# Performance work log

Measured on AMD Instinct MI355X. Metric: run time of the kernel, lower is better.

The kernel has to match this reference:

```python
import jax, jax.numpy as jnp
import numpy as np

K = 3  # kernel_size (stride=1, padding=0, same=False, entr=MAX_ENTROPY)


def setup_inputs() -> dict:
    key = jax.random.key(0)
    # Quantized values so global value-counts are non-trivial (mimics real NILM power readings)
    x = jax.random.randint(key, (8, 32, 256, 256), 0, 256).astype(jnp.float32)
    return {"x": x}


def _global_counts(x):
    """For each element, the number of occurrences of its value in the whole tensor
    (equivalent to torch.unique(return_inverse, return_counts) -> counts[inverse])."""
    flat = x.reshape(-1)
    n = flat.shape[0]
    order = jnp.argsort(flat)
    sv = flat[order]
    # group id increments at each value boundary in sorted order
    new_grp = jnp.concatenate([jnp.ones((1,), jnp.int32), (sv[1:] != sv[:-1]).astype(jnp.int32)])
    gid = jnp.cumsum(new_grp) - 1
    grp_counts = jax.ops.segment_sum(jnp.ones((n,), jnp.int32), gid, num_segments=n)
    counts_sorted = grp_counts[gid]
    counts = jnp.zeros((n,), jnp.int32).at[order].set(counts_sorted)
    return counts.reshape(x.shape)


def _windows(a, ho, wo):
    # [B,C,Ho,Wo,K*K]; (di,dj) row-major matches torch unfold(2).unfold(3).view(...,-1)
    return jnp.stack([a[:, :, di:di + ho, dj:dj + wo] for di in range(K) for dj in range(K)], axis=-1)


def reference(x):
    B, C, H, W = x.shape
    ho, wo = H - K + 1, W - K + 1
    probs = _global_counts(x)                 # int32 counts, detached in original
    pw = _windows(probs, ho, wo)              # [B,C,Ho,Wo,9]
    xw = _windows(x, ho, wo)                  # [B,C,Ho,Wo,9]
    # MAX_ENTROPY: pick the value with the minimum global count in each window
    idx = jnp.argmin(pw, axis=-1)             # first minimum, same as torch.min
    pool = jnp.take_along_axis(xw, idx[..., None], axis=-1)[..., 0]
    return pool                               # [B,C,Ho,Wo]
```

## Files before the change

kernel.cpp:

```cpp
#include <hip/hip_runtime.h>

#define B_   8
#define C_   32
#define H_   256
#define W_   256
#define BC_  (B_ * C_)
#define HO_  (H_ - 2)
#define WO_  (W_ - 2)
#define NIN_  (BC_ * H_ * W_)
#define NBINS 256
#define HCOLS 16
#define HBLOCKS 1024

__device__ __align__(8) int g_hist[NBINS];
__device__ int g_part[HBLOCKS * NBINS];

__global__ void zero_hist_kernel() { g_hist[threadIdx.x] = 0; }

__global__ __launch_bounds__(256) void hist_kernel(const float* __restrict__ x) {
    __shared__ int sh[NBINS * HCOLS];
    const int t = threadIdx.x;
    for (int i = t; i < NBINS * HCOLS; i += 256) sh[i] = 0;
    __syncthreads();

    const int col = t & (HCOLS - 1);
    const float4* x4 = (const float4*)x;
    const int stride = HBLOCKS * 256;
    float4 v[8];
#pragma unroll
    for (int half = 0; half < 2; ++half) {
        const int base = blockIdx.x * 256 + t + half * 8 * stride;
#pragma unroll
        for (int k = 0; k < 8; ++k) v[k] = x4[base + k * stride];
#pragma unroll
        for (int k = 0; k < 8; ++k) {
            atomicAdd(&sh[((int)v[k].x) * HCOLS + col], 1);
            atomicAdd(&sh[((int)v[k].y) * HCOLS + col], 1);
            atomicAdd(&sh[((int)v[k].z) * HCOLS + col], 1);
            atomicAdd(&sh[((int)v[k].w) * HCOLS + col], 1);
        }
    }
    __syncthreads();

    int s0 = 0;
#pragma unroll
    for (int c = 0; c < HCOLS; ++c) {
        const int cc = (c + t) & (HCOLS - 1);
        s0 += sh[t * HCOLS + cc];
    }
    g_part[blockIdx.x * NBINS + t] = s0;
}

__global__ __launch_bounds__(256) void reduce_kernel() {
    const int t = threadIdx.x;
    const int r0 = blockIdx.x * (HBLOCKS / 8);
    int s = 0;
#pragma unroll 8
    for (int i = 0; i < HBLOCKS / 8; ++i) s += g_part[(r0 + i) * NBINS + t];
    atomicAdd(&g_hist[t], s);
}

__global__ __launch_bounds__(256) void pool_kernel(const float* __restrict__ x,
                                                   float* __restrict__ out) {
    __shared__ int key_s[NBINS];
    __shared__ int tile[18 * W_];
    const int t = threadIdx.x;
    key_s[t] = (g_hist[t] << 8) | t;
    __syncthreads();

    const int bc = blockIdx.x >> 4;
    const int s  = blockIdx.x & 15;
    const int r0 = s * 16;
    const int rows_out = (r0 + 16 <= HO_) ? 16 : (HO_ - r0);
    const int rows_in  = rows_out + 2;

    const float4* xin = (const float4*)(x + ((long long)bc * H_ + r0) * W_);
    const int nf4 = rows_in * (W_ / 4);
    for (int idx = t; idx < nf4; idx += 256) {
        float4 v = xin[idx];
        int4 k;
        k.x = key_s[(int)v.x];
        k.y = key_s[(int)v.y];
        k.z = key_s[(int)v.z];
        k.w = key_s[(int)v.w];
        ((int4*)tile)[idx] = k;
    }
    __syncthreads();

    if (t >= WO_) return;

    int a0 = tile[t],        a1 = tile[t + 1],        a2 = tile[t + 2];
    int b0 = tile[W_ + t],   b1 = tile[W_ + t + 1],   b2 = tile[W_ + t + 2];
    float* orow = out + ((long long)bc * HO_ + r0) * WO_ + t;
    for (int r = 0; r < rows_out; ++r) {
        const int base = (r + 2) * W_ + t;
        const int c0 = tile[base], c1 = tile[base + 1], c2 = tile[base + 2];
        int best = a0, bm = a0 & ~255;
#define CAND(kk) { const int m = (kk) & ~255; if (m < bm) { bm = m; best = (kk); } }
        CAND(a1) CAND(a2) CAND(b0) CAND(b1) CAND(b2) CAND(c0) CAND(c1) CAND(c2)
#undef CAND
        orow[(long long)r * WO_] = (float)(best & 255);
        a0 = b0; a1 = b1; a2 = b2;
        b0 = c0; b1 = c1; b2 = c2;
    }
}

extern "C" void kernel_launch(void* const* d_in, const int* in_sizes, int n_in,
                              void* d_out, int out_size, void* d_ws, size_t ws_size,
                              hipStream_t stream) {
    const float* x = (const float*)d_in[0];
    float* out = (float*)d_out;
    (void)d_ws; (void)ws_size;

    zero_hist_kernel<<<1, NBINS, 0, stream>>>();
    hist_kernel<<<HBLOCKS, 256, 0, stream>>>(x);
    reduce_kernel<<<8, 256, 0, stream>>>();
    pool_kernel<<<BC_ * 16, 256, 0, stream>>>(x, out);
}
```

Measured before the change: 132.8 us.

## Cache input as packed bytes during histogram pass and reread in pool kernel

The histogram kernel now also writes each float4 as four packed 8-bit values into a global buffer, and the pool kernel reads that quarter-size buffer instead of the original float input. The reduction is folded into one 1024-thread block that writes the histogram directly, which drops the zeroing kernel and the global atomics. This trades an extra 16 MB write in the histogram pass for a 4x smaller read in the pool pass, plus one fewer launch. It relies on the input values being integers in 0..255, the same assumption the existing histogram already makes.

```diff
diff --git a/kernel.cpp b/kernel.cpp
--- a/kernel.cpp
+++ b/kernel.cpp
@@ -14,8 +14,7 @@
 
 __device__ __align__(8) int g_hist[NBINS];
 __device__ int g_part[HBLOCKS * NBINS];
-
-__global__ void zero_hist_kernel() { g_hist[threadIdx.x] = 0; }
+__device__ unsigned g_x8[NIN_ / 4];
 
 __global__ __launch_bounds__(256) void hist_kernel(const float* __restrict__ x) {
     __shared__ int sh[NBINS * HCOLS];
@@ -34,10 +33,13 @@
         for (int k = 0; k < 8; ++k) v[k] = x4[base + k * stride];
 #pragma unroll
         for (int k = 0; k < 8; ++k) {
-            atomicAdd(&sh[((int)v[k].x) * HCOLS + col], 1);
-            atomicAdd(&sh[((int)v[k].y) * HCOLS + col], 1);
-            atomicAdd(&sh[((int)v[k].z) * HCOLS + col], 1);
-            atomicAdd(&sh[((int)v[k].w) * HCOLS + col], 1);
+            const int ax = (int)v[k].x, ay = (int)v[k].y, az = (int)v[k].z, aw = (int)v[k].w;
+            g_x8[base + k * stride] =
+                (unsigned)ax | ((unsigned)ay << 8) | ((unsigned)az << 16) | ((unsigned)aw << 24);
+            atomicAdd(&sh[ax * HCOLS + col], 1);
+            atomicAdd(&sh[ay * HCOLS + col], 1);
+            atomicAdd(&sh[az * HCOLS + col], 1);
+            atomicAdd(&sh[aw * HCOLS + col], 1);
         }
     }
     __syncthreads();
@@ -51,17 +53,20 @@
     g_part[blockIdx.x * NBINS + t] = s0;
 }
 
-__global__ __launch_bounds__(256) void reduce_kernel() {
+__global__ __launch_bounds__(1024) void reduce_kernel() {
+    __shared__ int acc[4 * NBINS];
     const int t = threadIdx.x;
-    const int r0 = blockIdx.x * (HBLOCKS / 8);
+    const int bin = t & (NBINS - 1);
+    const int seg = t >> 8;
     int s = 0;
-#pragma unroll 8
-    for (int i = 0; i < HBLOCKS / 8; ++i) s += g_part[(r0 + i) * NBINS + t];
-    atomicAdd(&g_hist[t], s);
+#pragma unroll 16
+    for (int r = seg * 256; r < seg * 256 + 256; ++r) s += g_part[r * NBINS + bin];
+    acc[seg * NBINS + bin] = s;
+    __syncthreads();
+    if (t < NBINS) g_hist[t] = acc[t] + acc[NBINS + t] + acc[2 * NBINS + t] + acc[3 * NBINS + t];
 }
 
-__global__ __launch_bounds__(256) void pool_kernel(const float* __restrict__ x,
-                                                   float* __restrict__ out) {
+__global__ __launch_bounds__(256) void pool_kernel(float* __restrict__ out) {
     __shared__ int key_s[NBINS];
     __shared__ int tile[18 * W_];
     const int t = threadIdx.x;
@@ -74,15 +79,15 @@
     const int rows_out = (r0 + 16 <= HO_) ? 16 : (HO_ - r0);
     const int rows_in  = rows_out + 2;
 
-    const float4* xin = (const float4*)(x + ((long long)bc * H_ + r0) * W_);
-    const int nf4 = rows_in * (W_ / 4);
-    for (int idx = t; idx < nf4; idx += 256) {
-        float4 v = xin[idx];
+    const unsigned* xin = g_x8 + ((long long)bc * H_ + r0) * (W_ / 4);
+    const int nw = rows_in * (W_ / 4);
+    for (int idx = t; idx < nw; idx += 256) {
+        const unsigned u = xin[idx];
         int4 k;
-        k.x = key_s[(int)v.x];
-        k.y = key_s[(int)v.y];
-        k.z = key_s[(int)v.z];
-        k.w = key_s[(int)v.w];
+        k.x = key_s[u & 255];
+        k.y = key_s[(u >> 8) & 255];
+        k.z = key_s[(u >> 16) & 255];
+        k.w = key_s[u >> 24];
         ((int4*)tile)[idx] = k;
     }
     __syncthreads();
@@ -112,8 +117,7 @@
     float* out = (float*)d_out;
     (void)d_ws; (void)ws_size;
 
-    zero_hist_kernel<<<1, NBINS, 0, stream>>>();
     hist_kernel<<<HBLOCKS, 256, 0, stream>>>(x);
-    reduce_kernel<<<8, 256, 0, stream>>>();
-    pool_kernel<<<BC_ * 16, 256, 0, stream>>>(x, out);
+    reduce_kernel<<<1, 1024, 0, stream>>>();
+    pool_kernel<<<BC_ * 16, 256, 0, stream>>>(out);
 }
```

Measured after the change: 142.9 us. 7.6% more time.

## Fuse histogram and pooling into one cooperative kernel with grid sync

Applied to the files above, without the earlier changes.

Replaces the separate histogram, reduce and pool kernels with a single cooperative kernel of 256 blocks of 1024 threads, one block per image. Each block histograms its own image and atomically adds the result into 32 partial rows, then waits on a grid-wide sync, sums the partials and pools the same image. The image is read again after the sync, which may hit in L2/MALL, and launch overhead is reduced. In exchange, only 256 large blocks run, one per CU on mi355x, which lowers occupancy and parallelism for the pooling phase. The grid barrier adds its own cost.

```diff
diff --git a/kernel.cpp b/kernel.cpp
--- a/kernel.cpp
+++ b/kernel.cpp
@@ -1,4 +1,7 @@
 #include <hip/hip_runtime.h>
+#include <hip/hip_cooperative_groups.h>
+
+namespace cg = cooperative_groups;
 
 #define B_   8
 #define C_   32
@@ -7,31 +10,36 @@
 #define BC_  (B_ * C_)
 #define HO_  (H_ - 2)
 #define WO_  (W_ - 2)
-#define NIN_  (BC_ * H_ * W_)
 #define NBINS 256
 #define HCOLS 16
-#define HBLOCKS 1024
+#define PROWS 32
 
-__device__ __align__(8) int g_hist[NBINS];
-__device__ int g_part[HBLOCKS * NBINS];
+__device__ int g_part[PROWS * NBINS];
 
-__global__ void zero_hist_kernel() { g_hist[threadIdx.x] = 0; }
+__global__ __launch_bounds__(1024) void zero_part_kernel() {
+    const int t = threadIdx.x;
+#pragma unroll
+    for (int i = 0; i < (PROWS * NBINS) / 1024; ++i) g_part[i * 1024 + t] = 0;
+}
 
-__global__ __launch_bounds__(256) void hist_kernel(const float* __restrict__ x) {
-    __shared__ int sh[NBINS * HCOLS];
+__global__ __launch_bounds__(1024) void fused_kernel(const float* __restrict__ x,
+                                                     float* __restrict__ out) {
+    __shared__ int tile[18 * W_];
+    __shared__ int key_s[NBINS];
     const int t = threadIdx.x;
-    for (int i = t; i < NBINS * HCOLS; i += 256) sh[i] = 0;
+    const int bc = blockIdx.x;
+    const float4* ximg = (const float4*)(x + (long long)bc * H_ * W_);
+
+    int* sh = tile;
+    for (int i = t; i < NBINS * HCOLS; i += 1024) sh[i] = 0;
     __syncthreads();
 
     const int col = t & (HCOLS - 1);
-    const float4* x4 = (const float4*)x;
-    const int stride = HBLOCKS * 256;
-    float4 v[8];
 #pragma unroll
     for (int half = 0; half < 2; ++half) {
-        const int base = blockIdx.x * 256 + t + half * 8 * stride;
+        float4 v[8];
 #pragma unroll
-        for (int k = 0; k < 8; ++k) v[k] = x4[base + k * stride];
+        for (int k = 0; k < 8; ++k) v[k] = ximg[t + (half * 8 + k) * 1024];
 #pragma unroll
         for (int k = 0; k < 8; ++k) {
             atomicAdd(&sh[((int)v[k].x) * HCOLS + col], 1);
@@ -42,66 +50,64 @@
     }
     __syncthreads();
 
-    int s0 = 0;
+    if (t < NBINS) {
+        int s0 = 0;
 #pragma unroll
-    for (int c = 0; c < HCOLS; ++c) {
-        const int cc = (c + t) & (HCOLS - 1);
-        s0 += sh[t * HCOLS + cc];
+        for (int c = 0; c < HCOLS; ++c)
+            s0 += sh[t * HCOLS + ((c + t) & (HCOLS - 1))];
+        atomicAdd(&g_part[(bc & (PROWS - 1)) * NBINS + t], s0);
     }
-    g_part[blockIdx.x * NBINS + t] = s0;
-}
 
-__global__ __launch_bounds__(256) void reduce_kernel() {
-    const int t = threadIdx.x;
-    const int r0 = blockIdx.x * (HBLOCKS / 8);
-    int s = 0;
-#pragma unroll 8
-    for (int i = 0; i < HBLOCKS / 8; ++i) s += g_part[(r0 + i) * NBINS + t];
-    atomicAdd(&g_hist[t], s);
-}
+    cg::this_grid().sync();
 
-__global__ __launch_bounds__(256) void pool_kernel(const float* __restrict__ x,
-                                                   float* __restrict__ out) {
-    __shared__ int key_s[NBINS];
-    __shared__ int tile[18 * W_];
-    const int t = threadIdx.x;
-    key_s[t] = (g_hist[t] << 8) | t;
-    __syncthreads();
-
-    const int bc = blockIdx.x >> 4;
-    const int s  = blockIdx.x & 15;
-    const int r0 = s * 16;
-    const int rows_out = (r0 + 16 <= HO_) ? 16 : (HO_ - r0);
-    const int rows_in  = rows_out + 2;
-
-    const float4* xin = (const float4*)(x + ((long long)bc * H_ + r0) * W_);
-    const int nf4 = rows_in * (W_ / 4);
-    for (int idx = t; idx < nf4; idx += 256) {
-        float4 v = xin[idx];
-        int4 k;
-        k.x = key_s[(int)v.x];
-        k.y = key_s[(int)v.y];
-        k.z = key_s[(int)v.z];
-        k.w = key_s[(int)v.w];
-        ((int4*)tile)[idx] = k;
+    if (t < NBINS) {
+        int g = 0;
+#pragma unroll
+        for (int r = 0; r < PROWS; ++r) g += g_part[r * NBINS + t];
+        key_s[t] = (g << 8) | t;
     }
     __syncthreads();
 
-    if (t >= WO_) return;
+    const int cidx = t & 255;
+    const int rg   = t >> 8;
+    for (int s = 0; s < 16; ++s) {
+        const int r0 = s * 16;
+        const int rows_out = (s == 15) ? 14 : 16;
+        const int rows_in  = rows_out + 2;
 
-    int a0 = tile[t],        a1 = tile[t + 1],        a2 = tile[t + 2];
-    int b0 = tile[W_ + t],   b1 = tile[W_ + t + 1],   b2 = tile[W_ + t + 2];
-    float* orow = out + ((long long)bc * HO_ + r0) * WO_ + t;
-    for (int r = 0; r < rows_out; ++r) {
-        const int base = (r + 2) * W_ + t;
-        const int c0 = tile[base], c1 = tile[base + 1], c2 = tile[base + 2];
-        int best = a0, bm = a0 & ~255;
+        const float4* xrow = (const float4*)(x + ((long long)bc * H_ + r0) * W_);
+        const int nf4 = rows_in * (W_ / 4);
+        for (int idx = t; idx < nf4; idx += 1024) {
+            float4 v = xrow[idx];
+            int4 k;
+            k.x = key_s[(int)v.x];
+            k.y = key_s[(int)v.y];
+            k.z = key_s[(int)v.z];
+            k.w = key_s[(int)v.w];
+            ((int4*)tile)[idx] = k;
+        }
+        __syncthreads();
+
+        const int rbase = rg * 4;
+        const int rcnt = (rows_out - rbase < 4) ? (rows_out - rbase) : 4;
+        if (cidx < WO_ && rcnt > 0) {
+            const int* tp = tile + cidx;
+            int a0 = tp[rbase * W_],       a1 = tp[rbase * W_ + 1],       a2 = tp[rbase * W_ + 2];
+            int b0 = tp[(rbase + 1) * W_], b1 = tp[(rbase + 1) * W_ + 1], b2 = tp[(rbase + 1) * W_ + 2];
+            float* orow = out + ((long long)bc * HO_ + r0 + rbase) * WO_ + cidx;
+            for (int r = 0; r < rcnt; ++r) {
+                const int cb = (rbase + 2 + r) * W_;
+                const int c0 = tp[cb], c1 = tp[cb + 1], c2 = tp[cb + 2];
+                int best = a0, bm = a0 & ~255;
 #define CAND(kk) { const int m = (kk) & ~255; if (m < bm) { bm = m; best = (kk); } }
-        CAND(a1) CAND(a2) CAND(b0) CAND(b1) CAND(b2) CAND(c0) CAND(c1) CAND(c2)
+                CAND(a1) CAND(a2) CAND(b0) CAND(b1) CAND(b2) CAND(c0) CAND(c1) CAND(c2)
 #undef CAND
-        orow[(long long)r * WO_] = (float)(best & 255);
-        a0 = b0; a1 = b1; a2 = b2;
-        b0 = c0; b1 = c1; b2 = c2;
+                orow[(long long)r * WO_] = (float)(best & 255);
+                a0 = b0; a1 = b1; a2 = b2;
+                b0 = c0; b1 = c1; b2 = c2;
+            }
+        }
+        __syncthreads();
     }
 }
 
@@ -112,8 +118,9 @@
     float* out = (float*)d_out;
     (void)d_ws; (void)ws_size;
 
-    zero_hist_kernel<<<1, NBINS, 0, stream>>>();
-    hist_kernel<<<HBLOCKS, 256, 0, stream>>>(x);
-    reduce_kernel<<<8, 256, 0, stream>>>();
-    pool_kernel<<<BC_ * 16, 256, 0, stream>>>(x, out);
+    zero_part_kernel<<<1, 1024, 0, stream>>>();
+
+    void* args[] = { (void*)&x, (void*)&out };
+    hipLaunchCooperativeKernel((const void*)fused_kernel, dim3(BC_), dim3(1024),
+                               args, 0, stream);
 }
```

Measured after the change: 188.8 us. 1.42x slower.

## Vectorize pool window min with branchless keys and single-block histogram reduce

Applied to the files above, without the earlier changes.

Removes the zero-hist launch by reducing the partial histograms in one 1024-thread block that writes final counts directly, with no atomics. The pool kernel issues all global loads up front and stores keys into a padded int4 tile. Each thread now computes four output columns over a band of rows using branchless min over keys, where a window-position tag is ORed into bits 8-11 so ties still resolve to the first minimum. Outputs go out as nontemporal float2 stores. This trades more registers per thread for fewer launches and less shared-memory traffic and branching. It relies on count<<12 not overflowing, which holds for this input size.

```diff
diff --git a/kernel.cpp b/kernel.cpp
--- a/kernel.cpp
+++ b/kernel.cpp
@@ -11,11 +11,12 @@
 #define NBINS 256
 #define HCOLS 16
 #define HBLOCKS 1024
+#define TW4  65
+
+typedef float f2v __attribute__((ext_vector_type(2)));
 
 __device__ __align__(8) int g_hist[NBINS];
 __device__ int g_part[HBLOCKS * NBINS];
-
-__global__ void zero_hist_kernel() { g_hist[threadIdx.x] = 0; }
 
 __global__ __launch_bounds__(256) void hist_kernel(const float* __restrict__ x) {
     __shared__ int sh[NBINS * HCOLS];
@@ -44,64 +45,85 @@
 
     int s0 = 0;
 #pragma unroll
-    for (int c = 0; c < HCOLS; ++c) {
-        const int cc = (c + t) & (HCOLS - 1);
-        s0 += sh[t * HCOLS + cc];
-    }
+    for (int c = 0; c < HCOLS; ++c) s0 += sh[t * HCOLS + ((c + t) & (HCOLS - 1))];
     g_part[blockIdx.x * NBINS + t] = s0;
 }
 
-__global__ __launch_bounds__(256) void reduce_kernel() {
+__global__ __launch_bounds__(1024) void reduce_kernel() {
+    __shared__ int acc[4 * NBINS];
     const int t = threadIdx.x;
-    const int r0 = blockIdx.x * (HBLOCKS / 8);
+    const int bin = t & (NBINS - 1);
+    const int seg = t >> 8;
     int s = 0;
-#pragma unroll 8
-    for (int i = 0; i < HBLOCKS / 8; ++i) s += g_part[(r0 + i) * NBINS + t];
-    atomicAdd(&g_hist[t], s);
+#pragma unroll 16
+    for (int r = seg * 256; r < seg * 256 + 256; ++r) s += g_part[r * NBINS + bin];
+    acc[seg * NBINS + bin] = s;
+    __syncthreads();
+    if (t < NBINS) g_hist[t] = acc[t] + acc[NBINS + t] + acc[2 * NBINS + t] + acc[3 * NBINS + t];
 }
 
 __global__ __launch_bounds__(256) void pool_kernel(const float* __restrict__ x,
                                                    float* __restrict__ out) {
     __shared__ int key_s[NBINS];
-    __shared__ int tile[18 * W_];
+    __shared__ int4 tile[18 * TW4];
     const int t = threadIdx.x;
-    key_s[t] = (g_hist[t] << 8) | t;
+    key_s[t] = (g_hist[t] << 12) | t;
     __syncthreads();
 
     const int bc = blockIdx.x >> 4;
     const int s  = blockIdx.x & 15;
     const int r0 = s * 16;
-    const int rows_out = (r0 + 16 <= HO_) ? 16 : (HO_ - r0);
+    const int rows_out = (s == 15) ? 14 : 16;
     const int rows_in  = rows_out + 2;
+    const int nf4 = rows_in * (W_ / 4);
 
     const float4* xin = (const float4*)(x + ((long long)bc * H_ + r0) * W_);
-    const int nf4 = rows_in * (W_ / 4);
-    for (int idx = t; idx < nf4; idx += 256) {
-        float4 v = xin[idx];
-        int4 k;
-        k.x = key_s[(int)v.x];
-        k.y = key_s[(int)v.y];
-        k.z = key_s[(int)v.z];
-        k.w = key_s[(int)v.w];
-        ((int4*)tile)[idx] = k;
-    }
+    float4 v0 = xin[t], v1 = xin[t + 256], v2 = xin[t + 512], v3 = xin[t + 768];
+    const bool tail = (t + 1024) < nf4;
+    float4 v4;
+    if (tail) v4 = xin[t + 1024];
+
+#define PUT(i, v) { int4 k;                                                   \
+        k.x = key_s[(int)(v).x]; k.y = key_s[(int)(v).y];                     \
+        k.z = key_s[(int)(v).z]; k.w = key_s[(int)(v).w];                     \
+        tile[((i) >> 6) * TW4 + ((i) & 63)] = k; }
+    PUT(t, v0) PUT(t + 256, v1) PUT(t + 512, v2) PUT(t + 768, v3)
+    if (tail) PUT(t + 1024, v4)
+#undef PUT
     __syncthreads();
 
-    if (t >= WO_) return;
+    const int tc = t & 63;
+    const int tr = t >> 6;
+    const int o0 = tr * 4;
+    const int rcnt = (rows_out - o0 < 4) ? (rows_out - o0) : 4;
+    const int4* tp = tile + tc;
 
-    int a0 = tile[t],        a1 = tile[t + 1],        a2 = tile[t + 2];
-    int b0 = tile[W_ + t],   b1 = tile[W_ + t + 1],   b2 = tile[W_ + t + 2];
-    float* orow = out + ((long long)bc * HO_ + r0) * WO_ + t;
-    for (int r = 0; r < rows_out; ++r) {
-        const int base = (r + 2) * W_ + t;
-        const int c0 = tile[base], c1 = tile[base + 1], c2 = tile[base + 2];
-        int best = a0, bm = a0 & ~255;
-#define CAND(kk) { const int m = (kk) & ~255; if (m < bm) { bm = m; best = (kk); } }
-        CAND(a1) CAND(a2) CAND(b0) CAND(b1) CAND(b2) CAND(c0) CAND(c1) CAND(c2)
-#undef CAND
-        orow[(long long)r * WO_] = (float)(best & 255);
-        a0 = b0; a1 = b1; a2 = b2;
-        b0 = c0; b1 = c1; b2 = c2;
+    int4 a0 = tp[o0 * TW4],       a1 = tp[o0 * TW4 + 1];
+    int4 b0 = tp[(o0 + 1) * TW4], b1 = tp[(o0 + 1) * TW4 + 1];
+    float* obase = out + ((long long)bc * HO_ + r0 + o0) * WO_ + 4 * tc;
+
+    for (int rr = 0; rr < rcnt; ++rr) {
+        int4 c0 = tp[(o0 + 2 + rr) * TW4], c1 = tp[(o0 + 2 + rr) * TW4 + 1];
+        const int A[6] = {a0.x, a0.y, a0.z, a0.w, a1.x, a1.y};
+        const int Bt[6] = {b0.x, b0.y, b0.z, b0.w, b1.x, b1.y};
+        const int Ct[6] = {c0.x, c0.y, c0.z, c0.w, c1.x, c1.y};
+        float res[4];
+#pragma unroll
+        for (int c = 0; c < 4; ++c) {
+            int m0 = min(min(A[c], A[c + 1] | 0x100), A[c + 2] | 0x200);
+            int m1 = min(min(Bt[c] | 0x300, Bt[c + 1] | 0x400), Bt[c + 2] | 0x500);
+            int m2 = min(min(Ct[c] | 0x600, Ct[c + 1] | 0x700), Ct[c + 2] | 0x800);
+            res[c] = (float)(min(min(m0, m1), m2) & 255);
+        }
+        float* orow = obase + (long long)rr * WO_;
+        f2v lo = { res[0], res[1] };
+        __builtin_nontemporal_store(lo, (f2v*)orow);
+        if (tc < 63) {
+            f2v hi = { res[2], res[3] };
+            __builtin_nontemporal_store(hi, (f2v*)(orow + 2));
+        }
+        a0 = b0; a1 = b1;
+        b0 = c0; b1 = c1;
     }
 }
 
@@ -112,8 +134,7 @@
     float* out = (float*)d_out;
     (void)d_ws; (void)ws_size;
 
-    zero_hist_kernel<<<1, NBINS, 0, stream>>>();
     hist_kernel<<<HBLOCKS, 256, 0, stream>>>(x);
-    reduce_kernel<<<8, 256, 0, stream>>>();
+    reduce_kernel<<<1, 1024, 0, stream>>>();
     pool_kernel<<<BC_ * 16, 256, 0, stream>>>(x, out);
 }
```

Result: slower. 152.0 us (+14.5%).
